# Performance work log

Measured on AMD Instinct MI355X. Metric: run time of the kernel, lower is better.

The kernel has to match this reference:

```python
import jax, jax.numpy as jnp
import numpy as np
import math

B, L, D, H = 16, 144, 512, 8
DH = D // H          # 64, equals structure feature dim
DS, HS = 64, 8       # structure sub-attention model dim / heads
DFF = 2048

def ln(x, g, b, eps=1e-6):
    m = jnp.mean(x, -1, keepdims=True)
    v = jnp.mean((x - m) ** 2, -1, keepdims=True)
    return (x - m) * jax.lax.rsqrt(v + eps) * g + b

def setup_inputs():
    key = jax.random.key(0)
    ks = iter(jax.random.split(key, 32))
    def w(shape, s=0.02):
        return jax.random.normal(next(ks), shape, jnp.float32) * s
    return {
        "inputs": jax.random.normal(next(ks), (B, L, D), jnp.float32),
        "structure": jax.random.normal(next(ks), (L * L, 4, B, DS), jnp.float32),
        "mask": jax.random.randint(next(ks), (B, L, L), 0, 2, jnp.int32),
        "g_att": jnp.ones((D,), jnp.float32), "b_att": jnp.zeros((D,), jnp.float32),
        "Wq": w((D, D)), "bq": jnp.zeros((D,), jnp.float32),
        "Wk": w((D, D)), "bk": jnp.zeros((D,), jnp.float32),
        "Wv": w((D, D)), "bv": jnp.zeros((D,), jnp.float32),
        "Wo": w((D, D)), "bo": jnp.zeros((D,), jnp.float32),
        "sWq": w((DS, DS)), "sbq": jnp.zeros((DS,), jnp.float32),
        "sWk": w((DS, DS)), "sbk": jnp.zeros((DS,), jnp.float32),
        "sWv": w((DS, DS)), "sbv": jnp.zeros((DS,), jnp.float32),
        "sWo": w((DS, DS)), "sbo": jnp.zeros((DS,), jnp.float32),
        "Wc": w((DS, DS, 4)), "bc": jnp.zeros((DS,), jnp.float32),
        "g_s": jnp.ones((DS,), jnp.float32), "b_s": jnp.zeros((DS,), jnp.float32),
        "g_ffn": jnp.ones((D,), jnp.float32), "b_ffn": jnp.zeros((D,), jnp.float32),
        "W1": w((D, DFF)), "b1": jnp.zeros((DFF,), jnp.float32),
        "W2": w((DFF, D)), "b2": jnp.zeros((D,), jnp.float32),
    }

def _forward(inputs, structure, mask, g_att, b_att, Wq, bq, Wk, bk, Wv, bv, Wo, bo,
             sWq, sbq, sWk, sbk, sWv, sbv, sWo, sbo, Wc, bc, g_s, b_s,
             g_ffn, b_ffn, W1, b1, W2, b2):
    x_norm = ln(inputs, g_att, b_att)

    # --- structure pipeline: [L*L,4,B,DS] -> (transpose(0,1),transpose(0,2)) -> [B,L*L,4,DS] -> [N,4,DS]
    N = B * L * L
    s = jnp.transpose(structure, (2, 0, 1, 3)).reshape(N, 4, DS)
    dsh = DS // HS
    def split_s(t):
        return t.reshape(N, 4, HS, dsh).transpose(0, 2, 1, 3)
    q = split_s(s @ sWq + sbq) / math.sqrt(dsh)
    k = split_s(s @ sWk + sbk)
    v = split_s(s @ sWv + sbv)
    attn = jax.nn.softmax(jnp.einsum('nhid,nhjd->nhij', q, k), -1)
    ctx = jnp.einsum('nhij,nhjd->nhid', attn, v).transpose(0, 2, 1, 3).reshape(N, 4, DS)
    sa = ctx @ sWo + sbo                                  # [N,4,DS]
    # Conv1d(64,64,kernel=4) over the length-4 axis (valid -> length 1) + ReLU
    conv = jax.nn.relu(jnp.einsum('ntc,oct->no', sa, Wc) + bc)  # [N,DS]
    R = ln(conv.reshape(B, L, L, DS), g_s, b_s)           # per-pair relation embeddings

    # --- relation-aware self-attention (structure added to keys and values)
    def split_h(t):
        return t.reshape(B, L, H, DH).transpose(0, 2, 1, 3)
    q = split_h(x_norm @ Wq + bq) / math.sqrt(DH)
    k = split_h(x_norm @ Wk + bk)
    v = split_h(x_norm @ Wv + bv)
    scores = jnp.einsum('bhid,bhjd->bhij', q, k) + jnp.einsum('bhid,bijd->bhij', q, R)
    scores = jnp.where(mask[:, None, :, :] != 0, jnp.float32(-1e18), scores)
    attn = jax.nn.softmax(scores, -1)
    ctx = jnp.einsum('bhij,bhjd->bhid', attn, v) + jnp.einsum('bhij,bijd->bhid', attn, R)
    ctx = ctx.transpose(0, 2, 1, 3).reshape(B, L, D)
    x = ctx @ Wo + bo + inputs

    # --- FFN (pre-LN, residual outside)
    h = jax.nn.relu(ln(x, g_ffn, b_ffn) @ W1 + b1)
    return h @ W2 + b2 + x

def reference(inputs, structure, mask, g_att, b_att, Wq, bq, Wk, bk, Wv, bv, Wo, bo,
              sWq, sbq, sWk, sbk, sWv, sbv, sWo, sbo, Wc, bc, g_s, b_s,
              g_ffn, b_ffn, W1, b1, W2, b2):
    return _forward(inputs, structure, mask, g_att, b_att, Wq, bq, Wk, bk, Wv, bv, Wo, bo,
                    sWq, sbq, sWk, sbk, sWv, sbv, sWo, sbo, Wc, bc, g_s, b_s,
                    g_ffn, b_ffn, W1, b1, W2, b2)
```

## Files before the change

### kernel.cpp

```cpp
#include <hip/hip_runtime.h>
#include <math.h>


typedef __bf16 bf16_t;
typedef __bf16 bf16x8 __attribute__((ext_vector_type(8)));
typedef __bf16 bf16x4 __attribute__((ext_vector_type(4)));
typedef __bf16 bf16x2v __attribute__((ext_vector_type(2)));
typedef float f32x4 __attribute__((ext_vector_type(4)));

__global__ __launch_bounds__(256) void transpose_all(
    const float* __restrict__ Wq, const float* __restrict__ Wk,
    const float* __restrict__ Wv, const float* __restrict__ Wo,
    const float* __restrict__ W1, const float* __restrict__ W2,
    bf16_t* __restrict__ WqkvT, bf16_t* __restrict__ WoT,
    bf16_t* __restrict__ W1T, bf16_t* __restrict__ W2T) {
  int bid = blockIdx.x;
  const float* W; bf16_t* WT; int K, N; float scale = 1.f; int tile;
  if (bid < 256)       { W = Wq; WT = WqkvT;            K = 512;  N = 512;  scale = 0.125f; tile = bid; }
  else if (bid < 512)  { W = Wk; WT = WqkvT + 262144;   K = 512;  N = 512;  tile = bid - 256; }
  else if (bid < 768)  { W = Wv; WT = WqkvT + 524288;   K = 512;  N = 512;  tile = bid - 512; }
  else if (bid < 1024) { W = Wo; WT = WoT;              K = 512;  N = 512;  tile = bid - 768; }
  else if (bid < 2048) { W = W1; WT = W1T;              K = 512;  N = 2048; tile = bid - 1024; }
  else                 { W = W2; WT = W2T;              K = 2048; N = 512;  tile = bid - 2048; }
  int ntn = N >> 5;
  int nb = (tile % ntn) * 32, kb = (tile / ntn) * 32;
  __shared__ float t32[32][33];
  int tx = threadIdx.x & 31, ty = threadIdx.x >> 5;
#pragma unroll
  for (int i = ty; i < 32; i += 8) t32[i][tx] = W[(size_t)(kb + i) * N + nb + tx];
  __syncthreads();
#pragma unroll
  for (int i = ty; i < 32; i += 8)
    WT[(size_t)(nb + i) * K + kb + tx] = (__bf16)(t32[tx][i] * scale);
}

__global__ __launch_bounds__(256) void precompute_misc(
    const float* __restrict__ sWq, const float* __restrict__ sWk,
    const float* __restrict__ sWv, const float* __restrict__ sWo,
    const float* __restrict__ sbq, const float* __restrict__ sbk,
    const float* __restrict__ sbv, const float* __restrict__ sbo,
    const float* __restrict__ Wc, const float* __restrict__ bc,
    const float* __restrict__ bq, const float* __restrict__ bk,
    const float* __restrict__ bv, bf16_t* __restrict__ WT3,
    bf16_t* __restrict__ M2T, float* __restrict__ C0,
    float* __restrict__ sbqkv, float* __restrict__ bqkv) {
  int blk = blockIdx.x, tid = threadIdx.x;
  if (blk == 16) {
    const float qs = 0.35355339059327373f;
    for (int idx = tid; idx < 4096; idx += 256) {
      int j = idx >> 6, ic = idx & 63;
      int cj = (j & 7) * 8 + 2 * ((j >> 4) & 3) + ((j >> 3) & 1);
      WT3[idx] = (__bf16)(sWq[ic * 64 + cj] * qs);
      WT3[4096 + idx] = (__bf16)sWk[ic * 64 + cj];
      WT3[8192 + idx] = (__bf16)sWv[ic * 64 + cj];
    }
    if (tid < 64) {
      float s = bc[tid];
      for (int c = 0; c < 64; ++c) {
        float sb = sbo[c];
#pragma unroll
        for (int t = 0; t < 4; ++t) s += sb * Wc[tid * 256 + c * 4 + t];
      }
      C0[tid] = s;
      int cj = (tid & 7) * 8 + 2 * ((tid >> 4) & 3) + ((tid >> 3) & 1);
      sbqkv[tid] = sbq[cj] * qs;
      sbqkv[64 + tid] = sbk[cj];
      sbqkv[128 + tid] = sbv[cj];
    }
  } else if (blk == 17) {
    for (int i = tid; i < 1536; i += 256)
      bqkv[i] = (i < 512) ? bq[i] * 0.125f
                          : ((i < 1024) ? bk[i - 512] : bv[i - 1024]);
  } else {
    int t = blk >> 2;
    int e = (blk & 3) * 16 + (tid >> 4);
    int o4 = (tid & 15) * 4;
    float acc[4] = {0.f, 0.f, 0.f, 0.f};
    for (int c = 0; c < 64; ++c) {
      float a = sWo[e * 64 + c];
#pragma unroll
      for (int j = 0; j < 4; ++j) acc[j] += a * Wc[(o4 + j) * 256 + c * 4 + t];
    }
#pragma unroll
    for (int j = 0; j < 4; ++j)
      M2T[(o4 + j) * 256 + t * 64 + e] = (__bf16)acc[j];
  }
}

__global__ __launch_bounds__(256) void ln512(
    const float* __restrict__ x, const float* __restrict__ g,
    const float* __restrict__ bb, bf16_t* __restrict__ out) {
  int row = blockIdx.x, tid = threadIdx.x;
  const float* xr = x + (size_t)row * 512;
  float2 v = *(const float2*)&xr[tid * 2];
  float s1 = v.x + v.y;
  float s2 = v.x * v.x + v.y * v.y;
#pragma unroll
  for (int m = 32; m >= 1; m >>= 1) {
    s1 += __shfl_xor(s1, m);
    s2 += __shfl_xor(s2, m);
  }
  __shared__ float red[8];
  int wid = tid >> 6;
  if ((tid & 63) == 0) { red[wid * 2] = s1; red[wid * 2 + 1] = s2; }
  __syncthreads();
  s1 = red[0] + red[2] + red[4] + red[6];
  s2 = red[1] + red[3] + red[5] + red[7];
  float mean = s1 * (1.f / 512.f);
  float var = s2 * (1.f / 512.f) - mean * mean;
  float rs = 1.f / sqrtf(var + 1e-6f);
  int c = tid * 2;
  float2 gg = *(const float2*)&g[c];
  float2 bv = *(const float2*)&bb[c];
  bf16x2v o;
  o[0] = (__bf16)((v.x - mean) * rs * gg.x + bv.x);
  o[1] = (__bf16)((v.y - mean) * rs * gg.y + bv.y);
  *(bf16x2v*)&out[(size_t)row * 512 + c] = o;
}

__global__ __launch_bounds__(256) void gemm_bf16(
    const bf16_t* __restrict__ A, const bf16_t* __restrict__ BT,
    const float* __restrict__ bias, const float* __restrict__ res,
    float* __restrict__ Cf, bf16_t* __restrict__ Cb, int M, int N, int K,
    int relu) {
  int tid = threadIdx.x;
  int w = tid >> 6, l = tid & 63, l15 = l & 15, l4 = l >> 4;
  int n0 = blockIdx.x * 64, m0 = blockIdx.y * 64;
  int r = m0 + w * 16 + l15;
  const bf16_t* Arow = A + (size_t)r * K + l4 * 8;
  const bf16_t* Bbase = BT + (size_t)(n0 + l15) * K + l4 * 8;
  f32x4 acc[4];
#pragma unroll
  for (int ct = 0; ct < 4; ++ct) {
    float bv = bias[n0 + ct * 16 + l15];
    acc[ct] = (f32x4){bv, bv, bv, bv};
  }
#pragma unroll 4
  for (int k0 = 0; k0 < K; k0 += 32) {
    bf16x8 a8 = *(const bf16x8*)(Arow + k0);
#pragma unroll
    for (int ct = 0; ct < 4; ++ct) {
      bf16x8 b8 = *(const bf16x8*)(Bbase + (size_t)ct * 16 * K + k0);
      acc[ct] = __builtin_amdgcn_mfma_f32_16x16x32_bf16(a8, b8, acc[ct], 0, 0, 0);
    }
  }
#pragma unroll
  for (int ct = 0; ct < 4; ++ct) {
    int col = n0 + ct * 16 + l15;
#pragma unroll
    for (int i = 0; i < 4; ++i) {
      int row = m0 + w * 16 + l4 * 4 + i;
      float vv = acc[ct][i];
      if (relu) vv = fmaxf(vv, 0.f);
      if (res) vv += res[(size_t)row * N + col];
      if (Cf) Cf[(size_t)row * N + col] = vv;
      if (Cb) Cb[(size_t)row * N + col] = (__bf16)vv;
    }
  }
}

__global__ __launch_bounds__(256, 2) void struct_mfma(
    const float* __restrict__ S, const bf16_t* __restrict__ WT3,
    const float* __restrict__ sbqkv, const bf16_t* __restrict__ M2T,
    const float* __restrict__ C0, const float* __restrict__ gs,
    const float* __restrict__ bsv, bf16_t* __restrict__ Rout) {
  __shared__ __align__(16) char smem[67584];
  int tid = threadIdx.x;
  int w = tid >> 6, l = tid & 63, l15 = l & 15, l4 = l >> 4;
  int p0 = blockIdx.x * 4;

  bf16x8 wq[4][2], wk[4][2], wv[4][2];
  float biq[4], bik[4], biv[4];
#pragma unroll
  for (int ct = 0; ct < 4; ++ct) {
    int j = ct * 16 + l15;
#pragma unroll
    for (int kb = 0; kb < 2; ++kb) {
      int off = j * 64 + kb * 32 + l4 * 8;
      wq[ct][kb] = *(const bf16x8*)(WT3 + off);
      wk[ct][kb] = *(const bf16x8*)(WT3 + 4096 + off);
      wv[ct][kb] = *(const bf16x8*)(WT3 + 8192 + off);
    }
    biq[ct] = sbqkv[j];
    bik[ct] = sbqkv[64 + j];
    biv[ct] = sbqkv[128 + j];
  }

  {
    int row = tid >> 4;
    int cb0 = (tid & 15) * 16;
    const float* src = S + (size_t)(p0 * 4 + row) * 1024;
    int key = (row & 7) << 4;
#pragma unroll
    for (int i = 0; i < 8; ++i) {
      int colb = cb0 + i * 256;
      int c0 = colb >> 1;
      float4 u0 = *(const float4*)(src + c0);
      float4 u1 = *(const float4*)(src + c0 + 4);
      bf16x8 a;
      a[0] = (__bf16)u0.x; a[1] = (__bf16)u0.y;
      a[2] = (__bf16)u0.z; a[3] = (__bf16)u0.w;
      a[4] = (__bf16)u1.x; a[5] = (__bf16)u1.y;
      a[6] = (__bf16)u1.z; a[7] = (__bf16)u1.w;
      *(bf16x8*)(smem + row * 2048 + (colb ^ key)) = a;
    }
  }
  __syncthreads();

  int pl = l >> 4, h = l & 7, hi = (l >> 3) & 1;
#pragma unroll 1
  for (int r = 0; r < 4; ++r) {
    int b = r * 4 + w;
    int akey = (l15 & 7) << 4;
    int colb0 = b * 128 + l4 * 16;
    bf16x8 af0 = *(const bf16x8*)(smem + l15 * 2048 + (colb0 ^ akey));
    bf16x8 af1 = *(const bf16x8*)(smem + l15 * 2048 + ((colb0 + 64) ^ akey));
    f32x4 aq[4], ak[4], av[4];
#pragma unroll
    for (int ct = 0; ct < 4; ++ct) {
      aq[ct] = (f32x4){biq[ct], biq[ct], biq[ct], biq[ct]};
      ak[ct] = (f32x4){bik[ct], bik[ct], bik[ct], bik[ct]};
      av[ct] = (f32x4){biv[ct], biv[ct], biv[ct], biv[ct]};
    }
#pragma unroll
    for (int ct = 0; ct < 4; ++ct) {
      aq[ct] = __builtin_amdgcn_mfma_f32_16x16x32_bf16(af0, wq[ct][0], aq[ct], 0, 0, 0);
      aq[ct] = __builtin_amdgcn_mfma_f32_16x16x32_bf16(af1, wq[ct][1], aq[ct], 0, 0, 0);
      ak[ct] = __builtin_amdgcn_mfma_f32_16x16x32_bf16(af0, wk[ct][0], ak[ct], 0, 0, 0);
      ak[ct] = __builtin_amdgcn_mfma_f32_16x16x32_bf16(af1, wk[ct][1], ak[ct], 0, 0, 0);
      av[ct] = __builtin_amdgcn_mfma_f32_16x16x32_bf16(af0, wv[ct][0], av[ct], 0, 0, 0);
      av[ct] = __builtin_amdgcn_mfma_f32_16x16x32_bf16(af1, wv[ct][1], av[ct], 0, 0, 0);
    }
    float Sm[4][4];
#pragma unroll
    for (int i2 = 0; i2 < 4; ++i2)
#pragma unroll
      for (int j2 = 0; j2 < 4; ++j2)
        Sm[i2][j2] = aq[0][i2] * ak[0][j2] + aq[1][i2] * ak[1][j2] +
                     aq[2][i2] * ak[2][j2] + aq[3][i2] * ak[3][j2];
#pragma unroll
    for (int i2 = 0; i2 < 4; ++i2)
#pragma unroll
      for (int j2 = 0; j2 < 4; ++j2)
        Sm[i2][j2] += __shfl_xor(Sm[i2][j2], 8);
    float P[4][4], inv[4];
#pragma unroll
    for (int i2 = 0; i2 < 4; ++i2) {
      float rs = 0.f;
#pragma unroll
      for (int j2 = 0; j2 < 4; ++j2) {
        P[i2][j2] = __expf(Sm[i2][j2]);
        rs += P[i2][j2];
      }
      inv[i2] = __builtin_amdgcn_rcpf(rs);
    }
    int unit = r * 16 + w * 4 + pl;
    char* cb = smem + 32768 + unit * 544;
    int ckey = (unit & 7) << 4;
#pragma unroll
    for (int ct = 0; ct < 4; ++ct) {
      int c = h * 8 + 2 * ct + hi;
#pragma unroll
      for (int i2 = 0; i2 < 4; ++i2) {
        float cx = (P[i2][0] * av[ct][0] + P[i2][1] * av[ct][1] +
                    P[i2][2] * av[ct][2] + P[i2][3] * av[ct][3]) * inv[i2];
        *(bf16_t*)(cb + ((i2 * 128 + c * 2) ^ ckey)) = (__bf16)cx;
      }
    }
  }
  __syncthreads();

  float* cvp = (float*)smem;
  {
    bf16x8 ax[8];
    int rkey = (l15 & 7) << 4;
    char* cbase = smem + 32768 + (w * 16 + l15) * 544;
#pragma unroll
    for (int kb = 0; kb < 8; ++kb) {
      int byt = (kb >> 1) * 128 + (kb & 1) * 64 + l4 * 16;
      ax[kb] = *(const bf16x8*)(cbase + (byt ^ rkey));
    }
#pragma unroll 1
    for (int ct = 0; ct < 4; ++ct) {
      int o = ct * 16 + l15;
      float c0v = C0[o];
      f32x4 acc = (f32x4){c0v, c0v, c0v, c0v};
#pragma unroll
      for (int kb = 0; kb < 8; ++kb) {
        bf16x8 mf = *(const bf16x8*)(M2T + o * 256 + kb * 32 + l4 * 8);
        acc = __builtin_amdgcn_mfma_f32_16x16x32_bf16(ax[kb], mf, acc, 0, 0, 0);
      }
#pragma unroll
      for (int i2 = 0; i2 < 4; ++i2)
        cvp[(w * 16 + l4 * 4 + i2) * 68 + o] = fmaxf(acc[i2], 0.f);
    }
  }
  __syncthreads();

  {
    int unit = tid >> 2, ch0 = (tid & 3) * 16;
    const float* cr = cvp + unit * 68 + ch0;
    float4 v0 = *(const float4*)(cr);
    float4 v1 = *(const float4*)(cr + 4);
    float4 v2 = *(const float4*)(cr + 8);
    float4 v3 = *(const float4*)(cr + 12);
    float s1 = v0.x + v0.y + v0.z + v0.w + v1.x + v1.y + v1.z + v1.w +
               v2.x + v2.y + v2.z + v2.w + v3.x + v3.y + v3.z + v3.w;
    float s2 = v0.x * v0.x + v0.y * v0.y + v0.z * v0.z + v0.w * v0.w +
               v1.x * v1.x + v1.y * v1.y + v1.z * v1.z + v1.w * v1.w +
               v2.x * v2.x + v2.y * v2.y + v2.z * v2.z + v2.w * v2.w +
               v3.x * v3.x + v3.y * v3.y + v3.z * v3.z + v3.w * v3.w;
    s1 += __shfl_xor(s1, 1); s1 += __shfl_xor(s1, 2);
    s2 += __shfl_xor(s2, 1); s2 += __shfl_xor(s2, 2);
    float mean = s1 * (1.f / 64.f);
    float var = s2 * (1.f / 64.f) - mean * mean;
    float rstd = 1.f / sqrtf(var + 1e-6f);
    float4 g0 = *(const float4*)&gs[ch0];
    float4 g1 = *(const float4*)&gs[ch0 + 4];
    float4 g2 = *(const float4*)&gs[ch0 + 8];
    float4 g3 = *(const float4*)&gs[ch0 + 12];
    float4 b0 = *(const float4*)&bsv[ch0];
    float4 b1 = *(const float4*)&bsv[ch0 + 4];
    float4 b2 = *(const float4*)&bsv[ch0 + 8];
    float4 b3 = *(const float4*)&bsv[ch0 + 12];
    bf16x8 o0, o1;
    o0[0] = (__bf16)((v0.x - mean) * rstd * g0.x + b0.x);
    o0[1] = (__bf16)((v0.y - mean) * rstd * g0.y + b0.y);
    o0[2] = (__bf16)((v0.z - mean) * rstd * g0.z + b0.z);
    o0[3] = (__bf16)((v0.w - mean) * rstd * g0.w + b0.w);
    o0[4] = (__bf16)((v1.x - mean) * rstd * g1.x + b1.x);
    o0[5] = (__bf16)((v1.y - mean) * rstd * g1.y + b1.y);
    o0[6] = (__bf16)((v1.z - mean) * rstd * g1.z + b1.z);
    o0[7] = (__bf16)((v1.w - mean) * rstd * g1.w + b1.w);
    o1[0] = (__bf16)((v2.x - mean) * rstd * g2.x + b2.x);
    o1[1] = (__bf16)((v2.y - mean) * rstd * g2.y + b2.y);
    o1[2] = (__bf16)((v2.z - mean) * rstd * g2.z + b2.z);
    o1[3] = (__bf16)((v2.w - mean) * rstd * g2.w + b2.w);
    o1[4] = (__bf16)((v3.x - mean) * rstd * g3.x + b3.x);
    o1[5] = (__bf16)((v3.y - mean) * rstd * g3.y + b3.y);
    o1[6] = (__bf16)((v3.z - mean) * rstd * g3.z + b3.z);
    o1[7] = (__bf16)((v3.w - mean) * rstd * g3.w + b3.w);
    int rr = unit >> 4, w2 = (unit >> 2) & 3, pu = unit & 3;
    int b = rr * 4 + w2;
    size_t base = ((size_t)b * 20736 + p0 + pu) * 64 + ch0;
    *(bf16x8*)&Rout[base] = o0;
    *(bf16x8*)&Rout[base + 8] = o1;
  }
}

__global__ __launch_bounds__(256) void attn_main(
    const float* __restrict__ qkv, const bf16_t* __restrict__ R,
    const int* __restrict__ msk, bf16_t* __restrict__ ctx_out) {
  const int L = 144;
  int blk = blockIdx.x;
  int b = blk / L, i = blk - b * L;
  int tid = threadIdx.x;
  __shared__ float RlT[64][149];
  __shared__ float scl[8][144];
  __shared__ float q8[512];
  const bf16_t* Rrow = R + ((size_t)(b * L + i)) * L * 64;
  for (int idx = tid; idx < 144 * 8; idx += 256) {
    int j = idx >> 3, d8 = (idx & 7) * 8;
    bf16x8 r8 = *(const bf16x8*)&Rrow[(size_t)j * 64 + d8];
#pragma unroll
    for (int e = 0; e < 8; ++e) RlT[d8 + e][j] = (float)r8[e];
  }
  if (tid < 128)
    *(float4*)&q8[tid * 4] =
        *(const float4*)&qkv[(size_t)(b * L + i) * 1536 + tid * 4];
  __syncthreads();
  const float* kb = qkv + (size_t)b * L * 1536 + 512;
  const int* mrow = msk + (size_t)(b * L + i) * 144;
  for (int idx = tid; idx < 8 * 144; idx += 256) {
    int h = idx / 144, j = idx - h * 144;
    const float* kr = kb + (size_t)j * 1536 + h * 64;
    float s = 0.f;
#pragma unroll
    for (int d0 = 0; d0 < 64; d0 += 4) {
      float4 kv = *(const float4*)&kr[d0];
      s += q8[h * 64 + d0 + 0] * (kv.x + RlT[d0 + 0][j]);
      s += q8[h * 64 + d0 + 1] * (kv.y + RlT[d0 + 1][j]);
      s += q8[h * 64 + d0 + 2] * (kv.z + RlT[d0 + 2][j]);
      s += q8[h * 64 + d0 + 3] * (kv.w + RlT[d0 + 3][j]);
    }
    if (mrow[j] != 0) s = -1e18f;
    scl[h][j] = s;
  }
  __syncthreads();
  int h = tid >> 5, l = tid & 31;
  float m = -3.4e38f;
  for (int j = l; j < 144; j += 32) m = fmaxf(m, scl[h][j]);
#pragma unroll
  for (int mm = 16; mm >= 1; mm >>= 1) m = fmaxf(m, __shfl_xor(m, mm));
  float sum = 0.f;
  for (int j = l; j < 144; j += 32) {
    float p = __expf(scl[h][j] - m);
    scl[h][j] = p;
    sum += p;
  }
#pragma unroll
  for (int mm = 16; mm >= 1; mm >>= 1) sum += __shfl_xor(sum, mm);
  float inv = 1.f / sum;
  __syncthreads();
  int d0 = l * 2;
  float a0 = 0.f, a1 = 0.f;
  const float* vb = qkv + (size_t)b * L * 1536 + 1024 + h * 64 + d0;
  for (int j = 0; j < 144; ++j) {
    float p = scl[h][j];
    float2 vv = *(const float2*)&vb[(size_t)j * 1536];
    a0 += p * (vv.x + RlT[d0][j]);
    a1 += p * (vv.y + RlT[d0 + 1][j]);
  }
  bf16x2v o;
  o[0] = (__bf16)(a0 * inv);
  o[1] = (__bf16)(a1 * inv);
  *(bf16x2v*)&ctx_out[(size_t)(b * L + i) * 512 + h * 64 + d0] = o;
}

extern "C" void kernel_launch(void* const* d_in, const int* in_sizes, int n_in,
                              void* d_out, int out_size, void* d_ws,
                              size_t ws_size, hipStream_t stream) {
  (void)in_sizes; (void)n_in; (void)out_size; (void)ws_size;
  const float* inputs = (const float*)d_in[0];
  const float* structure = (const float*)d_in[1];
  const int* mask = (const int*)d_in[2];
  const float* g_att = (const float*)d_in[3];
  const float* b_att = (const float*)d_in[4];
  const float* Wq = (const float*)d_in[5];
  const float* bq = (const float*)d_in[6];
  const float* Wk = (const float*)d_in[7];
  const float* bk = (const float*)d_in[8];
  const float* Wv = (const float*)d_in[9];
  const float* bv = (const float*)d_in[10];
  const float* Wo = (const float*)d_in[11];
  const float* bo = (const float*)d_in[12];
  const float* sWq = (const float*)d_in[13];
  const float* sbq = (const float*)d_in[14];
  const float* sWk = (const float*)d_in[15];
  const float* sbk = (const float*)d_in[16];
  const float* sWv = (const float*)d_in[17];
  const float* sbv = (const float*)d_in[18];
  const float* sWo = (const float*)d_in[19];
  const float* sbo = (const float*)d_in[20];
  const float* Wc = (const float*)d_in[21];
  const float* bc = (const float*)d_in[22];
  const float* g_s = (const float*)d_in[23];
  const float* b_s = (const float*)d_in[24];
  const float* g_ffn = (const float*)d_in[25];
  const float* b_ffn = (const float*)d_in[26];
  const float* W1 = (const float*)d_in[27];
  const float* b1 = (const float*)d_in[28];
  const float* W2 = (const float*)d_in[29];
  const float* b2 = (const float*)d_in[30];

  char* base = (char*)d_ws;
  bf16_t* Rw = (bf16_t*)base;
  float* qkvw = (float*)(base + 42467328);
  float* xw = (float*)(base + 56623104);
  bf16_t* xnb = (bf16_t*)(base + 61341696);
  bf16_t* ctxb = (bf16_t*)(base + 63700992);
  bf16_t* WqkvT = (bf16_t*)(base + 66060288);
  bf16_t* WoT = (bf16_t*)(base + 67633152);
  bf16_t* W1T = (bf16_t*)(base + 68157440);
  bf16_t* W2T = (bf16_t*)(base + 70254592);
  bf16_t* WT3 = (bf16_t*)(base + 72351744);
  bf16_t* M2T = (bf16_t*)(base + 72376320);
  float* C0w = (float*)(base + 72409088);
  float* sbqkv = (float*)(base + 72409344);
  float* bqkv = (float*)(base + 72410112);
  bf16_t* hb = (bf16_t*)qkvw;
  float* out = (float*)d_out;

  transpose_all<<<3072, 256, 0, stream>>>(Wq, Wk, Wv, Wo, W1, W2, WqkvT, WoT,
                                          W1T, W2T);
  precompute_misc<<<18, 256, 0, stream>>>(sWq, sWk, sWv, sWo, sbq, sbk, sbv,
                                          sbo, Wc, bc, bq, bk, bv, WT3, M2T,
                                          C0w, sbqkv, bqkv);
  ln512<<<2304, 256, 0, stream>>>(inputs, g_att, b_att, xnb);
  gemm_bf16<<<dim3(24, 36), 256, 0, stream>>>(xnb, WqkvT, bqkv, nullptr, qkvw,
                                              nullptr, 2304, 1536, 512, 0);
  struct_mfma<<<5184, 256, 0, stream>>>(structure, WT3, sbqkv, M2T, C0w, g_s,
                                        b_s, Rw);
  attn_main<<<2304, 256, 0, stream>>>(qkvw, Rw, mask, ctxb);
  gemm_bf16<<<dim3(8, 36), 256, 0, stream>>>(ctxb, WoT, bo, inputs, xw,
                                             nullptr, 2304, 512, 512, 0);
  ln512<<<2304, 256, 0, stream>>>(xw, g_ffn, b_ffn, xnb);
  gemm_bf16<<<dim3(32, 36), 256, 0, stream>>>(xnb, W1T, b1, nullptr, nullptr,
                                              hb, 2304, 2048, 512, 1);
  gemm_bf16<<<dim3(8, 36), 256, 0, stream>>>(hb, W2T, b2, xw, out, nullptr,
                                             2304, 512, 2048, 0);
}
```

Before: 570.8 us.

## Widen struct kernel to 512 threads and store K/V in bf16 for attention

The structure kernel now runs 512 threads per block. Each wave handles fewer batch slices, and the per-thread preloaded weight fragments are replaced by in-loop loads, which frees registers and allows higher occupancy. The QKV projection is split into a fp32 Q GEMM and a bf16 K/V GEMM, so attention reads half as many bytes for keys and values. The risks are extra weight loads inside the MFMA loop, one additional kernel launch, and reduced precision for K and V.

```diff
diff --git a/kernel.cpp b/kernel.cpp
--- a/kernel.cpp
+++ b/kernel.cpp
@@ -159,7 +159,7 @@
   }
 }
 
-__global__ __launch_bounds__(256, 2) void struct_mfma(
+__global__ __launch_bounds__(512, 4) void struct_mfma(
     const float* __restrict__ S, const bf16_t* __restrict__ WT3,
     const float* __restrict__ sbqkv, const bf16_t* __restrict__ M2T,
     const float* __restrict__ C0, const float* __restrict__ gs,
@@ -169,39 +169,35 @@
   int w = tid >> 6, l = tid & 63, l15 = l & 15, l4 = l >> 4;
   int p0 = blockIdx.x * 4;
 
-  bf16x8 wq[4][2], wk[4][2], wv[4][2];
   float biq[4], bik[4], biv[4];
 #pragma unroll
   for (int ct = 0; ct < 4; ++ct) {
     int j = ct * 16 + l15;
-#pragma unroll
-    for (int kb = 0; kb < 2; ++kb) {
-      int off = j * 64 + kb * 32 + l4 * 8;
-      wq[ct][kb] = *(const bf16x8*)(WT3 + off);
-      wk[ct][kb] = *(const bf16x8*)(WT3 + 4096 + off);
-      wv[ct][kb] = *(const bf16x8*)(WT3 + 8192 + off);
-    }
     biq[ct] = sbqkv[j];
     bik[ct] = sbqkv[64 + j];
     biv[ct] = sbqkv[128 + j];
   }
 
   {
-    int row = tid >> 4;
-    int cb0 = (tid & 15) * 16;
+    int row = tid >> 5;
+    int cb0 = (tid & 31) * 16;
     const float* src = S + (size_t)(p0 * 4 + row) * 1024;
     int key = (row & 7) << 4;
-#pragma unroll
-    for (int i = 0; i < 8; ++i) {
-      int colb = cb0 + i * 256;
-      int c0 = colb >> 1;
-      float4 u0 = *(const float4*)(src + c0);
-      float4 u1 = *(const float4*)(src + c0 + 4);
+    float4 fu[4][2];
+#pragma unroll
+    for (int i = 0; i < 4; ++i) {
+      int c0 = (cb0 + i * 512) >> 1;
+      fu[i][0] = *(const float4*)(src + c0);
+      fu[i][1] = *(const float4*)(src + c0 + 4);
+    }
+#pragma unroll
+    for (int i = 0; i < 4; ++i) {
+      int colb = cb0 + i * 512;
       bf16x8 a;
-      a[0] = (__bf16)u0.x; a[1] = (__bf16)u0.y;
-      a[2] = (__bf16)u0.z; a[3] = (__bf16)u0.w;
-      a[4] = (__bf16)u1.x; a[5] = (__bf16)u1.y;
-      a[6] = (__bf16)u1.z; a[7] = (__bf16)u1.w;
+      a[0] = (__bf16)fu[i][0].x; a[1] = (__bf16)fu[i][0].y;
+      a[2] = (__bf16)fu[i][0].z; a[3] = (__bf16)fu[i][0].w;
+      a[4] = (__bf16)fu[i][1].x; a[5] = (__bf16)fu[i][1].y;
+      a[6] = (__bf16)fu[i][1].z; a[7] = (__bf16)fu[i][1].w;
       *(bf16x8*)(smem + row * 2048 + (colb ^ key)) = a;
     }
   }
@@ -209,8 +205,8 @@
 
   int pl = l >> 4, h = l & 7, hi = (l >> 3) & 1;
 #pragma unroll 1
-  for (int r = 0; r < 4; ++r) {
-    int b = r * 4 + w;
+  for (int r = 0; r < 2; ++r) {
+    int b = r * 8 + w;
     int akey = (l15 & 7) << 4;
     int colb0 = b * 128 + l4 * 16;
     bf16x8 af0 = *(const bf16x8*)(smem + l15 * 2048 + (colb0 ^ akey));
@@ -224,12 +220,19 @@
     }
 #pragma unroll
     for (int ct = 0; ct < 4; ++ct) {
-      aq[ct] = __builtin_amdgcn_mfma_f32_16x16x32_bf16(af0, wq[ct][0], aq[ct], 0, 0, 0);
-      aq[ct] = __builtin_amdgcn_mfma_f32_16x16x32_bf16(af1, wq[ct][1], aq[ct], 0, 0, 0);
-      ak[ct] = __builtin_amdgcn_mfma_f32_16x16x32_bf16(af0, wk[ct][0], ak[ct], 0, 0, 0);
-      ak[ct] = __builtin_amdgcn_mfma_f32_16x16x32_bf16(af1, wk[ct][1], ak[ct], 0, 0, 0);
-      av[ct] = __builtin_amdgcn_mfma_f32_16x16x32_bf16(af0, wv[ct][0], av[ct], 0, 0, 0);
-      av[ct] = __builtin_amdgcn_mfma_f32_16x16x32_bf16(af1, wv[ct][1], av[ct], 0, 0, 0);
+      int off = (ct * 16 + l15) * 64 + l4 * 8;
+      bf16x8 wq0 = *(const bf16x8*)(WT3 + off);
+      bf16x8 wq1 = *(const bf16x8*)(WT3 + off + 32);
+      bf16x8 wk0 = *(const bf16x8*)(WT3 + 4096 + off);
+      bf16x8 wk1 = *(const bf16x8*)(WT3 + 4096 + off + 32);
+      bf16x8 wv0 = *(const bf16x8*)(WT3 + 8192 + off);
+      bf16x8 wv1 = *(const bf16x8*)(WT3 + 8192 + off + 32);
+      aq[ct] = __builtin_amdgcn_mfma_f32_16x16x32_bf16(af0, wq0, aq[ct], 0, 0, 0);
+      aq[ct] = __builtin_amdgcn_mfma_f32_16x16x32_bf16(af1, wq1, aq[ct], 0, 0, 0);
+      ak[ct] = __builtin_amdgcn_mfma_f32_16x16x32_bf16(af0, wk0, ak[ct], 0, 0, 0);
+      ak[ct] = __builtin_amdgcn_mfma_f32_16x16x32_bf16(af1, wk1, ak[ct], 0, 0, 0);
+      av[ct] = __builtin_amdgcn_mfma_f32_16x16x32_bf16(af0, wv0, av[ct], 0, 0, 0);
+      av[ct] = __builtin_amdgcn_mfma_f32_16x16x32_bf16(af1, wv1, av[ct], 0, 0, 0);
     }
     float Sm[4][4];
 #pragma unroll
@@ -254,7 +257,7 @@
       }
       inv[i2] = __builtin_amdgcn_rcpf(rs);
     }
-    int unit = r * 16 + w * 4 + pl;
+    int unit = r * 32 + w * 4 + pl;
     char* cb = smem + 32768 + unit * 544;
     int ckey = (unit & 7) << 4;
 #pragma unroll
@@ -272,16 +275,18 @@
 
   float* cvp = (float*)smem;
   {
+    int g = w >> 1;
     bf16x8 ax[8];
     int rkey = (l15 & 7) << 4;
-    char* cbase = smem + 32768 + (w * 16 + l15) * 544;
+    char* cbase = smem + 32768 + (g * 16 + l15) * 544;
 #pragma unroll
     for (int kb = 0; kb < 8; ++kb) {
       int byt = (kb >> 1) * 128 + (kb & 1) * 64 + l4 * 16;
       ax[kb] = *(const bf16x8*)(cbase + (byt ^ rkey));
     }
 #pragma unroll 1
-    for (int ct = 0; ct < 4; ++ct) {
+    for (int cc = 0; cc < 2; ++cc) {
+      int ct = (w & 1) * 2 + cc;
       int o = ct * 16 + l15;
       float c0v = C0[o];
       f32x4 acc = (f32x4){c0v, c0v, c0v, c0v};
@@ -292,65 +297,48 @@
       }
 #pragma unroll
       for (int i2 = 0; i2 < 4; ++i2)
-        cvp[(w * 16 + l4 * 4 + i2) * 68 + o] = fmaxf(acc[i2], 0.f);
+        cvp[(g * 16 + l4 * 4 + i2) * 68 + o] = fmaxf(acc[i2], 0.f);
     }
   }
   __syncthreads();
 
   {
-    int unit = tid >> 2, ch0 = (tid & 3) * 16;
+    int unit = tid >> 3, ch0 = (tid & 7) * 8;
     const float* cr = cvp + unit * 68 + ch0;
     float4 v0 = *(const float4*)(cr);
     float4 v1 = *(const float4*)(cr + 4);
-    float4 v2 = *(const float4*)(cr + 8);
-    float4 v3 = *(const float4*)(cr + 12);
-    float s1 = v0.x + v0.y + v0.z + v0.w + v1.x + v1.y + v1.z + v1.w +
-               v2.x + v2.y + v2.z + v2.w + v3.x + v3.y + v3.z + v3.w;
+    float s1 = v0.x + v0.y + v0.z + v0.w + v1.x + v1.y + v1.z + v1.w;
     float s2 = v0.x * v0.x + v0.y * v0.y + v0.z * v0.z + v0.w * v0.w +
-               v1.x * v1.x + v1.y * v1.y + v1.z * v1.z + v1.w * v1.w +
-               v2.x * v2.x + v2.y * v2.y + v2.z * v2.z + v2.w * v2.w +
-               v3.x * v3.x + v3.y * v3.y + v3.z * v3.z + v3.w * v3.w;
-    s1 += __shfl_xor(s1, 1); s1 += __shfl_xor(s1, 2);
-    s2 += __shfl_xor(s2, 1); s2 += __shfl_xor(s2, 2);
+               v1.x * v1.x + v1.y * v1.y + v1.z * v1.z + v1.w * v1.w;
+    s1 += __shfl_xor(s1, 1); s1 += __shfl_xor(s1, 2); s1 += __shfl_xor(s1, 4);
+    s2 += __shfl_xor(s2, 1); s2 += __shfl_xor(s2, 2); s2 += __shfl_xor(s2, 4);
     float mean = s1 * (1.f / 64.f);
     float var = s2 * (1.f / 64.f) - mean * mean;
     float rstd = 1.f / sqrtf(var + 1e-6f);
     float4 g0 = *(const float4*)&gs[ch0];
     float4 g1 = *(const float4*)&gs[ch0 + 4];
-    float4 g2 = *(const float4*)&gs[ch0 + 8];
-    float4 g3 = *(const float4*)&gs[ch0 + 12];
     float4 b0 = *(const float4*)&bsv[ch0];
     float4 b1 = *(const float4*)&bsv[ch0 + 4];
-    float4 b2 = *(const float4*)&bsv[ch0 + 8];
-    float4 b3 = *(const float4*)&bsv[ch0 + 12];
-    bf16x8 o0, o1;
-    o0[0] = (__bf16)((v0.x - mean) * rstd * g0.x + b0.x);
-    o0[1] = (__bf16)((v0.y - mean) * rstd * g0.y + b0.y);
-    o0[2] = (__bf16)((v0.z - mean) * rstd * g0.z + b0.z);
-    o0[3] = (__bf16)((v0.w - mean) * rstd * g0.w + b0.w);
-    o0[4] = (__bf16)((v1.x - mean) * rstd * g1.x + b1.x);
-    o0[5] = (__bf16)((v1.y - mean) * rstd * g1.y + b1.y);
-    o0[6] = (__bf16)((v1.z - mean) * rstd * g1.z + b1.z);
-    o0[7] = (__bf16)((v1.w - mean) * rstd * g1.w + b1.w);
-    o1[0] = (__bf16)((v2.x - mean) * rstd * g2.x + b2.x);
-    o1[1] = (__bf16)((v2.y - mean) * rstd * g2.y + b2.y);
-    o1[2] = (__bf16)((v2.z - mean) * rstd * g2.z + b2.z);
-    o1[3] = (__bf16)((v2.w - mean) * rstd * g2.w + b2.w);
-    o1[4] = (__bf16)((v3.x - mean) * rstd * g3.x + b3.x);
-    o1[5] = (__bf16)((v3.y - mean) * rstd * g3.y + b3.y);
-    o1[6] = (__bf16)((v3.z - mean) * rstd * g3.z + b3.z);
-    o1[7] = (__bf16)((v3.w - mean) * rstd * g3.w + b3.w);
-    int rr = unit >> 4, w2 = (unit >> 2) & 3, pu = unit & 3;
-    int b = rr * 4 + w2;
+    bf16x8 ov;
+    ov[0] = (__bf16)((v0.x - mean) * rstd * g0.x + b0.x);
+    ov[1] = (__bf16)((v0.y - mean) * rstd * g0.y + b0.y);
+    ov[2] = (__bf16)((v0.z - mean) * rstd * g0.z + b0.z);
+    ov[3] = (__bf16)((v0.w - mean) * rstd * g0.w + b0.w);
+    ov[4] = (__bf16)((v1.x - mean) * rstd * g1.x + b1.x);
+    ov[5] = (__bf16)((v1.y - mean) * rstd * g1.y + b1.y);
+    ov[6] = (__bf16)((v1.z - mean) * rstd * g1.z + b1.z);
+    ov[7] = (__bf16)((v1.w - mean) * rstd * g1.w + b1.w);
+    int rr = unit >> 5, w8 = (unit >> 2) & 7, pu = unit & 3;
+    int b = rr * 8 + w8;
     size_t base = ((size_t)b * 20736 + p0 + pu) * 64 + ch0;
-    *(bf16x8*)&Rout[base] = o0;
-    *(bf16x8*)&Rout[base + 8] = o1;
+    *(bf16x8*)&Rout[base] = ov;
   }
 }
 
 __global__ __launch_bounds__(256) void attn_main(
-    const float* __restrict__ qkv, const bf16_t* __restrict__ R,
-    const int* __restrict__ msk, bf16_t* __restrict__ ctx_out) {
+    const float* __restrict__ q, const bf16_t* __restrict__ kv,
+    const bf16_t* __restrict__ R, const int* __restrict__ msk,
+    bf16_t* __restrict__ ctx_out) {
   const int L = 144;
   int blk = blockIdx.x;
   int b = blk / L, i = blk - b * L;
@@ -367,21 +355,25 @@
   }
   if (tid < 128)
     *(float4*)&q8[tid * 4] =
-        *(const float4*)&qkv[(size_t)(b * L + i) * 1536 + tid * 4];
-  __syncthreads();
-  const float* kb = qkv + (size_t)b * L * 1536 + 512;
+        *(const float4*)&q[(size_t)(b * L + i) * 512 + tid * 4];
+  __syncthreads();
+  const bf16_t* kb = kv + (size_t)b * L * 1024;
   const int* mrow = msk + (size_t)(b * L + i) * 144;
   for (int idx = tid; idx < 8 * 144; idx += 256) {
     int h = idx / 144, j = idx - h * 144;
-    const float* kr = kb + (size_t)j * 1536 + h * 64;
+    const bf16_t* kr = kb + (size_t)j * 1024 + h * 64;
     float s = 0.f;
 #pragma unroll
-    for (int d0 = 0; d0 < 64; d0 += 4) {
-      float4 kv = *(const float4*)&kr[d0];
-      s += q8[h * 64 + d0 + 0] * (kv.x + RlT[d0 + 0][j]);
-      s += q8[h * 64 + d0 + 1] * (kv.y + RlT[d0 + 1][j]);
-      s += q8[h * 64 + d0 + 2] * (kv.z + RlT[d0 + 2][j]);
-      s += q8[h * 64 + d0 + 3] * (kv.w + RlT[d0 + 3][j]);
+    for (int d0 = 0; d0 < 64; d0 += 8) {
+      bf16x8 k8 = *(const bf16x8*)&kr[d0];
+      s += q8[h * 64 + d0 + 0] * ((float)k8[0] + RlT[d0 + 0][j]);
+      s += q8[h * 64 + d0 + 1] * ((float)k8[1] + RlT[d0 + 1][j]);
+      s += q8[h * 64 + d0 + 2] * ((float)k8[2] + RlT[d0 + 2][j]);
+      s += q8[h * 64 + d0 + 3] * ((float)k8[3] + RlT[d0 + 3][j]);
+      s += q8[h * 64 + d0 + 4] * ((float)k8[4] + RlT[d0 + 4][j]);
+      s += q8[h * 64 + d0 + 5] * ((float)k8[5] + RlT[d0 + 5][j]);
+      s += q8[h * 64 + d0 + 6] * ((float)k8[6] + RlT[d0 + 6][j]);
+      s += q8[h * 64 + d0 + 7] * ((float)k8[7] + RlT[d0 + 7][j]);
     }
     if (mrow[j] != 0) s = -1e18f;
     scl[h][j] = s;
@@ -404,12 +396,12 @@
   __syncthreads();
   int d0 = l * 2;
   float a0 = 0.f, a1 = 0.f;
-  const float* vb = qkv + (size_t)b * L * 1536 + 1024 + h * 64 + d0;
+  const bf16_t* vb = kb + 512 + h * 64 + d0;
   for (int j = 0; j < 144; ++j) {
     float p = scl[h][j];
-    float2 vv = *(const float2*)&vb[(size_t)j * 1536];
-    a0 += p * (vv.x + RlT[d0][j]);
-    a1 += p * (vv.y + RlT[d0 + 1][j]);
+    bf16x2v vv = *(const bf16x2v*)&vb[(size_t)j * 1024];
+    a0 += p * ((float)vv[0] + RlT[d0][j]);
+    a1 += p * ((float)vv[1] + RlT[d0 + 1][j]);
   }
   bf16x2v o;
   o[0] = (__bf16)(a0 * inv);
@@ -455,7 +447,7 @@
 
   char* base = (char*)d_ws;
   bf16_t* Rw = (bf16_t*)base;
-  float* qkvw = (float*)(base + 42467328);
+  float* qw = (float*)(base + 42467328);
   float* xw = (float*)(base + 56623104);
   bf16_t* xnb = (bf16_t*)(base + 61341696);
   bf16_t* ctxb = (bf16_t*)(base + 63700992);
@@ -468,7 +460,8 @@
   float* C0w = (float*)(base + 72409088);
   float* sbqkv = (float*)(base + 72409344);
   float* bqkv = (float*)(base + 72410112);
-  bf16_t* hb = (bf16_t*)qkvw;
+  bf16_t* kvb = (bf16_t*)(base + 72416256);
+  bf16_t* hb = (bf16_t*)(base + 42467328 + 4718592);
   float* out = (float*)d_out;
 
   transpose_all<<<3072, 256, 0, stream>>>(Wq, Wk, Wv, Wo, W1, W2, WqkvT, WoT,
@@ -477,11 +470,14 @@
                                           sbo, Wc, bc, bq, bk, bv, WT3, M2T,
                                           C0w, sbqkv, bqkv);
   ln512<<<2304, 256, 0, stream>>>(inputs, g_att, b_att, xnb);
-  gemm_bf16<<<dim3(24, 36), 256, 0, stream>>>(xnb, WqkvT, bqkv, nullptr, qkvw,
-                                              nullptr, 2304, 1536, 512, 0);
-  struct_mfma<<<5184, 256, 0, stream>>>(structure, WT3, sbqkv, M2T, C0w, g_s,
+  gemm_bf16<<<dim3(8, 36), 256, 0, stream>>>(xnb, WqkvT, bqkv, nullptr, qw,
+                                             nullptr, 2304, 512, 512, 0);
+  gemm_bf16<<<dim3(16, 36), 256, 0, stream>>>(xnb, WqkvT + 262144, bqkv + 512,
+                                              nullptr, nullptr, kvb, 2304,
+                                              1024, 512, 0);
+  struct_mfma<<<5184, 512, 0, stream>>>(structure, WT3, sbqkv, M2T, C0w, g_s,
                                         b_s, Rw);
-  attn_main<<<2304, 256, 0, stream>>>(qkvw, Rw, mask, ctxb);
+  attn_main<<<2304, 256, 0, stream>>>(qw, kvb, Rw, mask, ctxb);
   gemm_bf16<<<dim3(8, 36), 256, 0, stream>>>(ctxb, WoT, bo, inputs, xw,
                                              nullptr, 2304, 512, 512, 0);
   ln512<<<2304, 256, 0, stream>>>(xw, g_ffn, b_ffn, xnb);
```

After: 913.9 us. +60.1%, slower.
